# Performance work log

Measured on AMD Instinct MI355X. Metric: run time of the kernel, lower is better.

## Reference

```python
import jax, jax.numpy as jnp
import numpy as np

B, N1, N2, H, LAT, MID = 16, 2048, 2048, 768, 128, 256


def setup_inputs() -> dict:
    key = jax.random.key(0)
    ks = jax.random.split(key, 20)
    def lin(k, n_in, n_out):
        s = 1.0 / np.sqrt(n_in)
        kw, kb = jax.random.split(k)
        W = jax.random.uniform(kw, (n_in, n_out), jnp.float32, -s, s)
        b = jax.random.uniform(kb, (n_out,), jnp.float32, -s, s)
        return W, b
    We1, be1 = lin(ks[0], H, MID)
    We2, be2 = lin(ks[1], MID, LAT)
    Wq, bq = lin(ks[2], LAT, LAT)
    Wk, bk = lin(ks[3], LAT, LAT)
    Wv, bv = lin(ks[4], LAT, LAT)
    Wd1, bd1 = lin(ks[5], LAT, MID)
    Wd2, bd2 = lin(ks[6], MID, H)
    main_feature = jax.random.normal(ks[7], (B, N1, H), jnp.float32)
    feature = jax.random.normal(ks[8], (B, N2, H), jnp.float32)
    return dict(main_feature=main_feature, feature=feature,
                We1=We1, be1=be1, We2=We2, be2=be2,
                Wq=Wq, bq=bq, Wk=Wk, bk=bk, Wv=Wv, bv=bv,
                Wd1=Wd1, bd1=bd1, Wd2=Wd2, bd2=bd2)


def reference(main_feature, feature, We1, be1, We2, be2, Wq, bq, Wk, bk, Wv, bv, Wd1, bd1, Wd2, bd2):
    def encode(x):
        h = jax.nn.relu(x @ We1 + be1)
        return jax.nn.relu(h @ We2 + be2)  # [B, N, LAT]

    def decode(x):
        h = jax.nn.relu(x @ Wd1 + bd1)
        return jax.nn.sigmoid(h @ Wd2 + bd2)  # [B, N, H]

    m = encode(main_feature)           # [B, N1, LAT]
    f = encode(feature)                # [B, N2, LAT]
    q = m @ Wq + bq                    # [B, N1, LAT]
    k = f @ Wk + bk                    # [B, N2, LAT]
    v = f @ Wv + bv                    # [B, N2, LAT]
    scores = jnp.einsum('bnd,bmd->bnm', q, k)   # unscaled, [B, N1, N2]
    probs = jax.nn.softmax(scores, axis=-1)
    attn = jnp.einsum('bnm,bmd->bnd', probs, v)  # [B, N1, LAT]
    return decode(attn)                # [B, N1, H]
```

## Files before the change

kernel.cpp:

```cpp
#include <hip/hip_runtime.h>
#include <stdint.h>

typedef unsigned short u16;
typedef __bf16 bf16x8 __attribute__((ext_vector_type(8)));
typedef float f32x4 __attribute__((ext_vector_type(4)));

#define MM   32768

__device__ __forceinline__ u16 f2bf(float f) {
    uint32_t u; __builtin_memcpy(&u, &f, 4);
    u += 0x7fffu + ((u >> 16) & 1u);
    return (u16)(u >> 16);
}

__device__ __forceinline__ void gl_lds16(const u16* g, u16* l) {
    __builtin_amdgcn_global_load_lds(
        (__attribute__((address_space(1))) void*)(g),
        (__attribute__((address_space(3))) void*)(l), 16, 0, 0);
}

__global__ void transpose_all(const float* __restrict__ We1, const float* __restrict__ We2,
                              const float* __restrict__ Wq,  const float* __restrict__ Wk,
                              const float* __restrict__ Wv,  const float* __restrict__ Wd1,
                              const float* __restrict__ Wd2, u16* __restrict__ wt) {
    int i = blockIdx.x * 256 + threadIdx.x;
    const float* src; int K, N, off;
    if      (i < 196608) { src = We1; K = 768; N = 256; off = i;          }
    else if (i < 229376) { src = We2; K = 256; N = 128; off = i - 196608; }
    else if (i < 245760) { src = Wq;  K = 128; N = 128; off = i - 229376; }
    else if (i < 262144) { src = Wk;  K = 128; N = 128; off = i - 245760; }
    else if (i < 278528) { src = Wv;  K = 128; N = 128; off = i - 262144; }
    else if (i < 311296) { src = Wd1; K = 128; N = 256; off = i - 278528; }
    else if (i < 507904) { src = Wd2; K = 256; N = 768; off = i - 311296; }
    else return;
    int n = off / K, k = off % K;
    wt[i] = f2bf(src[(size_t)k * N + n]);
}

template <int BM, int ACT, bool TRANS, bool A_F32, bool OUT_F32>
__global__ void gemm_bt(const void* __restrict__ Avp, const u16* __restrict__ Wt,
                        const float* __restrict__ bias, void* __restrict__ Cvp,
                        int M, int N, int K) {
    constexpr int MI  = BM / 32;
    constexpr int AF4 = BM / 16;
    __shared__ u16 a_sh[2][BM * 64];
    __shared__ u16 b_sh[2][128 * 64];
    const int t = threadIdx.x;
    const int wave = t >> 6, lane = t & 63;
    const int lrow = lane & 15, quad = lane >> 4;
    const int wr = wave >> 1, wc = wave & 1;
    const int m0 = blockIdx.x * BM, n0 = blockIdx.y * 128;

    const float* Af = (const float*)Avp;
    const u16*   Ab = (const u16*)Avp;

    f32x4 acc[MI][4];
#pragma unroll
    for (int i = 0; i < MI; i++)
#pragma unroll
        for (int j = 0; j < 4; j++) acc[i][j] = (f32x4){0.f, 0.f, 0.f, 0.f};

    float4 pf[A_F32 ? AF4 : 1];

    auto stage_b = [&](int buf, int k0) {
#pragma unroll
        for (int it = 0; it < 4; it++) {
            int s = it * 256 + t;
            gl_lds16(Wt + (size_t)(n0 + (s >> 3)) * K + k0 + (s & 7) * 8,
                     &b_sh[buf][(it * 256 + wave * 64) * 8]);
        }
    };
    auto stage_a_bf = [&](int buf, int k0) {
#pragma unroll
        for (int it = 0; it < BM / 32; it++) {
            int s = it * 256 + t;
            gl_lds16(Ab + (size_t)(m0 + (s >> 3)) * K + k0 + (s & 7) * 8,
                     &a_sh[buf][(it * 256 + wave * 64) * 8]);
        }
    };
    auto load_a_f32 = [&](int k0) {
#pragma unroll
        for (int it = 0; it < AF4; it++) {
            int s = it * 256 + t;
            pf[it] = *(const float4*)(Af + (size_t)(m0 + (s >> 4)) * K + k0 + (s & 15) * 4);
        }
    };
    auto write_a_f32 = [&](int buf) {
#pragma unroll
        for (int it = 0; it < AF4; it++) {
            int s = it * 256 + t;
            int row = s >> 4, kc = s & 15;
            float4 v = pf[it];
            uint32_t p0 = (uint32_t)f2bf(v.x) | ((uint32_t)f2bf(v.y) << 16);
            uint32_t p1 = (uint32_t)f2bf(v.z) | ((uint32_t)f2bf(v.w) << 16);
            *(uint32_t*)&a_sh[buf][row * 64 + kc * 4]     = p0;
            *(uint32_t*)&a_sh[buf][row * 64 + kc * 4 + 2] = p1;
        }
    };

    if (A_F32) { load_a_f32(0); write_a_f32(0); } else stage_a_bf(0, 0);
    stage_b(0, 0);
    __syncthreads();

    int cur = 0;
    for (int k0 = 0; k0 < K; k0 += 64) {
        const int nk = k0 + 64;
        if (nk < K) {
            if (A_F32) load_a_f32(nk); else stage_a_bf(cur ^ 1, nk);
            stage_b(cur ^ 1, nk);
        }
#pragma unroll
        for (int kk = 0; kk < 2; kk++) {
            bf16x8 af[MI], bfv[4];
#pragma unroll
            for (int i = 0; i < MI; i++)
                af[i] = *(const bf16x8*)&a_sh[cur][(wr * (BM / 2) + i * 16 + lrow) * 64 + kk * 32 + quad * 8];
#pragma unroll
            for (int j = 0; j < 4; j++)
                bfv[j] = *(const bf16x8*)&b_sh[cur][(wc * 64 + j * 16 + lrow) * 64 + kk * 32 + quad * 8];
#pragma unroll
            for (int i = 0; i < MI; i++)
#pragma unroll
                for (int j = 0; j < 4; j++)
                    acc[i][j] = __builtin_amdgcn_mfma_f32_16x16x32_bf16(af[i], bfv[j], acc[i][j], 0, 0, 0);
        }
        if (A_F32 && nk < K) write_a_f32(cur ^ 1);
        __syncthreads();
        cur ^= 1;
    }

    float bv4[4];
#pragma unroll
    for (int j = 0; j < 4; j++) bv4[j] = bias[n0 + wc * 64 + j * 16 + lrow];

#pragma unroll
    for (int i = 0; i < MI; i++) {
#pragma unroll
        for (int j = 0; j < 4; j++) {
            const int col = n0 + wc * 64 + j * 16 + lrow;
            if (!TRANS) {
#pragma unroll
                for (int r = 0; r < 4; r++) {
                    float x = acc[i][j][r] + bv4[j];
                    if (ACT == 1) x = fmaxf(x, 0.f);
                    if (ACT == 2) x = 1.f / (1.f + __expf(-x));
                    const int row = m0 + wr * (BM / 2) + i * 16 + quad * 4 + r;
                    if (OUT_F32) ((float*)Cvp)[(size_t)row * N + col] = x;
                    else         ((u16*)Cvp)[(size_t)row * N + col] = f2bf(x);
                }
            } else {
                u16 vv[4];
#pragma unroll
                for (int r = 0; r < 4; r++) vv[r] = f2bf(acc[i][j][r] + bv4[j]);
                u16* Cb = (u16*)Cvp;
                size_t base = (size_t)(m0 >> 11) * ((size_t)N * 2048) + (size_t)col * 2048 +
                              (m0 & 2047) + wr * (BM / 2) + i * 16 + quad * 4;
                *(uint32_t*)&Cb[base]     = (uint32_t)vv[0] | ((uint32_t)vv[1] << 16);
                *(uint32_t*)&Cb[base + 2] = (uint32_t)vv[2] | ((uint32_t)vv[3] << 16);
            }
        }
    }
}

__global__ __launch_bounds__(256)
void flash_attn(const u16* __restrict__ Q, const u16* __restrict__ Kb,
                const u16* __restrict__ VT, u16* __restrict__ O) {
    __shared__ u16 k_sh[64 * 128];
    __shared__ u16 v_sh[128 * 64];
    __shared__ u16 qp_sh[64 * 128];

    const int t = threadIdx.x, wave = t >> 6, lane = t & 63;
    const int lrow = lane & 15, quad = lane >> 4;
    const int lsw = (lrow & 7) << 3;
    const int b = blockIdx.x >> 5, q0 = (blockIdx.x & 31) * 64;

    const u16* qg = Q + (size_t)(b * 2048 + q0) * 128;
#pragma unroll
    for (int it = 0; it < 4; it++) {
        int s = it * 256 + t;
        int srcSeg = s ^ ((s >> 4) & 7);
        gl_lds16(qg + (size_t)srcSeg * 8, &qp_sh[(it * 256 + wave * 64) * 8]);
    }
    __syncthreads();
    bf16x8 qf[4];
#pragma unroll
    for (int ks = 0; ks < 4; ks++)
        qf[ks] = *(const bf16x8*)&qp_sh[(((wave * 16 + lrow) * 128) + ks * 32 + quad * 8) ^ lsw];

    f32x4 o_acc[8];
#pragma unroll
    for (int ct = 0; ct < 8; ct++) o_acc[ct] = (f32x4){0.f, 0.f, 0.f, 0.f};
    float m_i[4] = {-1e30f, -1e30f, -1e30f, -1e30f};
    float l_i[4] = {0.f, 0.f, 0.f, 0.f};

    for (int tile = 0; tile < 32; tile++) {
        const u16* kg = Kb + (size_t)(b * 2048 + tile * 64) * 128;
        const u16* vg = VT + (size_t)b * 262144 + tile * 64;
#pragma unroll
        for (int it = 0; it < 4; it++) {
            int s = it * 256 + t;
            int srcSeg = s ^ ((s >> 4) & 7);
            gl_lds16(kg + (size_t)srcSeg * 8, &k_sh[(it * 256 + wave * 64) * 8]);
        }
#pragma unroll
        for (int it = 0; it < 4; it++) {
            int s = it * 256 + t;
            int row = s >> 3, c = (s & 7) ^ (row & 7);
            gl_lds16(vg + (size_t)row * 2048 + c * 8,
                     &v_sh[(it * 256 + wave * 64) * 8]);
        }
        __syncthreads();

        f32x4 s_acc[4];
        __builtin_amdgcn_s_setprio(1);
#pragma unroll
        for (int ct = 0; ct < 4; ct++) {
            f32x4 a = (f32x4){0.f, 0.f, 0.f, 0.f};
#pragma unroll
            for (int ks = 0; ks < 4; ks++) {
                bf16x8 kf = *(const bf16x8*)&k_sh[(((ct * 16 + lrow) * 128) + ks * 32 + quad * 8) ^ lsw];
                a = __builtin_amdgcn_mfma_f32_16x16x32_bf16(qf[ks], kf, a, 0, 0, 0);
            }
            s_acc[ct] = a;
        }
        __builtin_amdgcn_s_setprio(0);

        float mnew[4], alpha[4], ps[4];
#pragma unroll
        for (int r = 0; r < 4; r++) {
            float mx = s_acc[0][r];
#pragma unroll
            for (int ct = 1; ct < 4; ct++) mx = fmaxf(mx, s_acc[ct][r]);
#pragma unroll
            for (int d = 8; d >= 1; d >>= 1) mx = fmaxf(mx, __shfl_xor(mx, d, 64));
            mnew[r] = fmaxf(m_i[r], mx);
            alpha[r] = __expf(m_i[r] - mnew[r]);
            m_i[r] = mnew[r];
            ps[r] = 0.f;
        }
#pragma unroll
        for (int ct = 0; ct < 4; ct++)
#pragma unroll
            for (int r = 0; r < 4; r++) {
                float p = __expf(s_acc[ct][r] - mnew[r]);
                ps[r] += p;
                qp_sh[(((wave * 16 + quad * 4 + r) * 128) + ct * 16 + lrow) ^ (((quad * 4 + r) & 7) << 3)] = f2bf(p);
            }
#pragma unroll
        for (int r = 0; r < 4; r++) {
#pragma unroll
            for (int d = 8; d >= 1; d >>= 1) ps[r] += __shfl_xor(ps[r], d, 64);
            l_i[r] = l_i[r] * alpha[r] + ps[r];
        }
#pragma unroll
        for (int ct = 0; ct < 8; ct++)
#pragma unroll
            for (int r = 0; r < 4; r++) o_acc[ct][r] *= alpha[r];

        bf16x8 pf[2];
#pragma unroll
        for (int ks = 0; ks < 2; ks++)
            pf[ks] = *(const bf16x8*)&qp_sh[(((wave * 16 + lrow) * 128) + ks * 32 + quad * 8) ^ lsw];
        __builtin_amdgcn_s_setprio(1);
#pragma unroll
        for (int ct = 0; ct < 8; ct++)
#pragma unroll
            for (int ks = 0; ks < 2; ks++) {
                bf16x8 vf = *(const bf16x8*)&v_sh[(((ct * 16 + lrow) * 64) + ks * 32 + quad * 8) ^ lsw];
                o_acc[ct] = __builtin_amdgcn_mfma_f32_16x16x32_bf16(pf[ks], vf, o_acc[ct], 0, 0, 0);
            }
        __builtin_amdgcn_s_setprio(0);
        __syncthreads();
    }

    float inv_l[4];
#pragma unroll
    for (int r = 0; r < 4; r++) inv_l[r] = 1.f / l_i[r];
#pragma unroll
    for (int ct = 0; ct < 8; ct++)
#pragma unroll
        for (int r = 0; r < 4; r++) {
            const int row = b * 2048 + q0 + wave * 16 + quad * 4 + r;
            O[(size_t)row * 128 + ct * 16 + lrow] = f2bf(o_acc[ct][r] * inv_l[r]);
        }
}

extern "C" void kernel_launch(void* const* d_in, const int* in_sizes, int n_in,
                              void* d_out, int out_size, void* d_ws, size_t ws_size,
                              hipStream_t stream) {
    const float* mainf = (const float*)d_in[0];
    const float* feat  = (const float*)d_in[1];
    const float* We1 = (const float*)d_in[2];  const float* be1 = (const float*)d_in[3];
    const float* We2 = (const float*)d_in[4];  const float* be2 = (const float*)d_in[5];
    const float* Wq  = (const float*)d_in[6];  const float* bq  = (const float*)d_in[7];
    const float* Wk  = (const float*)d_in[8];  const float* bk  = (const float*)d_in[9];
    const float* Wv  = (const float*)d_in[10]; const float* bv  = (const float*)d_in[11];
    const float* Wd1 = (const float*)d_in[12]; const float* bd1 = (const float*)d_in[13];
    const float* Wd2 = (const float*)d_in[14]; const float* bd2 = (const float*)d_in[15];

    u16* ws = (u16*)d_ws;
    u16* wt = ws;
    u16* h1 = wt + 524288;
    u16* mf = h1 + 8388608;
    u16* qb = mf + 4194304;
    u16* kb = qb + 4194304;
    u16* vT = kb + 4194304;
    u16* wt_e1 = wt, *wt_e2 = wt + 196608, *wt_q = wt + 229376, *wt_k = wt + 245760,
       * wt_v = wt + 262144, *wt_d1 = wt + 278528, *wt_d2 = wt + 311296;

    transpose_all<<<1984, 256, 0, stream>>>(We1, We2, Wq, Wk, Wv, Wd1, Wd2, wt);

    gemm_bt<64, 1, false, true,  false><<<dim3(512, 2), 256, 0, stream>>>(mainf, wt_e1, be1, h1, MM, 256, 768);
    gemm_bt<64, 1, false, false, false><<<dim3(512, 1), 256, 0, stream>>>(h1,    wt_e2, be2, mf, MM, 128, 256);
    gemm_bt<64, 0, false, false, false><<<dim3(512, 1), 256, 0, stream>>>(mf,    wt_q,  bq,  qb, MM, 128, 128);
    gemm_bt<64, 1, false, true,  false><<<dim3(512, 2), 256, 0, stream>>>(feat, wt_e1, be1, h1, MM, 256, 768);
    gemm_bt<64, 1, false, false, false><<<dim3(512, 1), 256, 0, stream>>>(h1,   wt_e2, be2, mf, MM, 128, 256);
    gemm_bt<64, 0, false, false, false><<<dim3(512, 1), 256, 0, stream>>>(mf,   wt_k,  bk,  kb, MM, 128, 128);
    gemm_bt<64, 0, true,  false, false><<<dim3(512, 1), 256, 0, stream>>>(mf,   wt_v,  bv,  vT, MM, 128, 128);

    flash_attn<<<512, 256, 0, stream>>>(qb, kb, vT, mf);

    gemm_bt<64, 1, false, false, false><<<dim3(512, 2), 256, 0, stream>>>(mf, wt_d1, bd1, h1, MM, 256, 128);
    gemm_bt<64, 2, false, false, true ><<<dim3(512, 6), 256, 0, stream>>>(h1, wt_d2, bd2, d_out, MM, 768, 256);
}
```

Baseline: 496.1 us.

## Double-buffer K tiles in flash attention and use fine-grained vmcnt waits in GEMM

The flash attention kernel now double-buffers the K tile and prefetches the next K tile, plus the next V tile, while the current tile is being computed. Explicit s_waitcnt vmcnt counts and raw barriers replace __syncthreads. The GEMM main loop is restructured the same way, with partial vmcnt waits so the next tile's global loads overlap the MFMA compute, and setprio is raised around the MFMA block. This targets load latency exposed at each barrier, at the cost of more LDS and fragile hand-tuned wait counts that can cause races if they are wrong.

```diff
diff --git a/kernel.cpp b/kernel.cpp
--- a/kernel.cpp
+++ b/kernel.cpp
@@ -6,6 +6,11 @@
 typedef float f32x4 __attribute__((ext_vector_type(4)));
 
 #define MM   32768
+
+#define WAITV(N) asm volatile("s_waitcnt vmcnt(" #N ")" ::: "memory")
+#define WAITL0() asm volatile("s_waitcnt lgkmcnt(0)" ::: "memory")
+#define BARR()   do { asm volatile("" ::: "memory"); __builtin_amdgcn_s_barrier(); \
+                      asm volatile("" ::: "memory"); } while (0)
 
 __device__ __forceinline__ u16 f2bf(float f) {
     uint32_t u; __builtin_memcpy(&u, &f, 4);
@@ -97,35 +102,58 @@
             *(uint32_t*)&a_sh[buf][row * 64 + kc * 4 + 2] = p1;
         }
     };
-
-    if (A_F32) { load_a_f32(0); write_a_f32(0); } else stage_a_bf(0, 0);
-    stage_b(0, 0);
-    __syncthreads();
+    auto compute = [&](int buf) {
+#pragma unroll
+        for (int kk = 0; kk < 2; kk++) {
+            bf16x8 af[MI], bfv[4];
+#pragma unroll
+            for (int i = 0; i < MI; i++)
+                af[i] = *(const bf16x8*)&a_sh[buf][(wr * (BM / 2) + i * 16 + lrow) * 64 + kk * 32 + quad * 8];
+#pragma unroll
+            for (int j = 0; j < 4; j++)
+                bfv[j] = *(const bf16x8*)&b_sh[buf][(wc * 64 + j * 16 + lrow) * 64 + kk * 32 + quad * 8];
+            __builtin_amdgcn_s_setprio(1);
+#pragma unroll
+            for (int i = 0; i < MI; i++)
+#pragma unroll
+                for (int j = 0; j < 4; j++)
+                    acc[i][j] = __builtin_amdgcn_mfma_f32_16x16x32_bf16(af[i], bfv[j], acc[i][j], 0, 0, 0);
+            __builtin_amdgcn_s_setprio(0);
+        }
+    };
+
+    const int T = K >> 6;
+    if (A_F32) {
+        load_a_f32(0); stage_b(0, 0);
+        WAITV(4);
+        write_a_f32(0);
+        WAITL0(); WAITV(0);
+    } else {
+        stage_a_bf(0, 0); stage_b(0, 0);
+        WAITV(0);
+    }
+    BARR();
 
     int cur = 0;
-    for (int k0 = 0; k0 < K; k0 += 64) {
-        const int nk = k0 + 64;
-        if (nk < K) {
+    for (int tt = 0; tt < T; ++tt) {
+        const int nk = (tt + 1) * 64;
+        const bool more = nk < K;
+        if (more) {
             if (A_F32) load_a_f32(nk); else stage_a_bf(cur ^ 1, nk);
             stage_b(cur ^ 1, nk);
         }
-#pragma unroll
-        for (int kk = 0; kk < 2; kk++) {
-            bf16x8 af[MI], bfv[4];
-#pragma unroll
-            for (int i = 0; i < MI; i++)
-                af[i] = *(const bf16x8*)&a_sh[cur][(wr * (BM / 2) + i * 16 + lrow) * 64 + kk * 32 + quad * 8];
-#pragma unroll
-            for (int j = 0; j < 4; j++)
-                bfv[j] = *(const bf16x8*)&b_sh[cur][(wc * 64 + j * 16 + lrow) * 64 + kk * 32 + quad * 8];
-#pragma unroll
-            for (int i = 0; i < MI; i++)
-#pragma unroll
-                for (int j = 0; j < 4; j++)
-                    acc[i][j] = __builtin_amdgcn_mfma_f32_16x16x32_bf16(af[i], bfv[j], acc[i][j], 0, 0, 0);
-        }
-        if (A_F32 && nk < K) write_a_f32(cur ^ 1);
-        __syncthreads();
+        if (tt > 0) {
+            if (more) { if (A_F32) { WAITV(8); } else { WAITV(6); } }
+            else      { WAITV(0); }
+            BARR();
+        }
+        compute(cur);
+        if (A_F32 && more) {
+            WAITV(4);
+            write_a_f32(cur ^ 1);
+            WAITL0();
+        }
+        if (more) BARR();
         cur ^= 1;
     }
 
@@ -165,7 +193,7 @@
 __global__ __launch_bounds__(256)
 void flash_attn(const u16* __restrict__ Q, const u16* __restrict__ Kb,
                 const u16* __restrict__ VT, u16* __restrict__ O) {
-    __shared__ u16 k_sh[64 * 128];
+    __shared__ u16 kb_sh[2][64 * 128];
     __shared__ u16 v_sh[128 * 64];
     __shared__ u16 qp_sh[64 * 128];
 
@@ -174,14 +202,27 @@
     const int lsw = (lrow & 7) << 3;
     const int b = blockIdx.x >> 5, q0 = (blockIdx.x & 31) * 64;
 
-    const u16* qg = Q + (size_t)(b * 2048 + q0) * 128;
+    int ksrc[4], vsrc[4], ldst[4];
 #pragma unroll
     for (int it = 0; it < 4; it++) {
         int s = it * 256 + t;
-        int srcSeg = s ^ ((s >> 4) & 7);
-        gl_lds16(qg + (size_t)srcSeg * 8, &qp_sh[(it * 256 + wave * 64) * 8]);
-    }
-    __syncthreads();
+        ksrc[it] = (s ^ ((s >> 4) & 7)) * 8;
+        int row = s >> 3, cc = (s & 7) ^ (row & 7);
+        vsrc[it] = row * 2048 + cc * 8;
+        ldst[it] = (it * 256 + wave * 64) * 8;
+    }
+
+    const u16* qg  = Q  + (size_t)(b * 2048 + q0) * 128;
+    const u16* kgb = Kb + (size_t)b * 2048 * 128;
+    const u16* vgb = VT + (size_t)b * 262144;
+
+#pragma unroll
+    for (int it = 0; it < 4; it++) gl_lds16(qg + ksrc[it], &qp_sh[ldst[it]]);
+#pragma unroll
+    for (int it = 0; it < 4; it++) gl_lds16(kgb + ksrc[it], &kb_sh[0][ldst[it]]);
+#pragma unroll
+    for (int it = 0; it < 4; it++) gl_lds16(vgb + vsrc[it], &v_sh[ldst[it]]);
+    WAITV(8); BARR();
     bf16x8 qf[4];
 #pragma unroll
     for (int ks = 0; ks < 4; ks++)
@@ -194,22 +235,11 @@
     float l_i[4] = {0.f, 0.f, 0.f, 0.f};
 
     for (int tile = 0; tile < 32; tile++) {
-        const u16* kg = Kb + (size_t)(b * 2048 + tile * 64) * 128;
-        const u16* vg = VT + (size_t)b * 262144 + tile * 64;
-#pragma unroll
-        for (int it = 0; it < 4; it++) {
-            int s = it * 256 + t;
-            int srcSeg = s ^ ((s >> 4) & 7);
-            gl_lds16(kg + (size_t)srcSeg * 8, &k_sh[(it * 256 + wave * 64) * 8]);
-        }
-#pragma unroll
-        for (int it = 0; it < 4; it++) {
-            int s = it * 256 + t;
-            int row = s >> 3, c = (s & 7) ^ (row & 7);
-            gl_lds16(vg + (size_t)row * 2048 + c * 8,
-                     &v_sh[(it * 256 + wave * 64) * 8]);
-        }
-        __syncthreads();
+        const int c = tile & 1;
+        const u16* kg_n = kgb + (size_t)(((tile + 1) & 31) * 64) * 128;
+#pragma unroll
+        for (int it = 0; it < 4; it++) gl_lds16(kg_n + ksrc[it], &kb_sh[c ^ 1][ldst[it]]);
+        WAITV(8); BARR();
 
         f32x4 s_acc[4];
         __builtin_amdgcn_s_setprio(1);
@@ -218,7 +248,7 @@
             f32x4 a = (f32x4){0.f, 0.f, 0.f, 0.f};
 #pragma unroll
             for (int ks = 0; ks < 4; ks++) {
-                bf16x8 kf = *(const bf16x8*)&k_sh[(((ct * 16 + lrow) * 128) + ks * 32 + quad * 8) ^ lsw];
+                bf16x8 kf = *(const bf16x8*)&kb_sh[c][(((ct * 16 + lrow) * 128) + ks * 32 + quad * 8) ^ lsw];
                 a = __builtin_amdgcn_mfma_f32_16x16x32_bf16(qf[ks], kf, a, 0, 0, 0);
             }
             s_acc[ct] = a;
@@ -257,20 +287,28 @@
 #pragma unroll
             for (int r = 0; r < 4; r++) o_acc[ct][r] *= alpha[r];
 
-        bf16x8 pf[2];
+        WAITV(4); BARR();
+
+        bf16x8 pfa[2];
 #pragma unroll
         for (int ks = 0; ks < 2; ks++)
-            pf[ks] = *(const bf16x8*)&qp_sh[(((wave * 16 + lrow) * 128) + ks * 32 + quad * 8) ^ lsw];
+            pfa[ks] = *(const bf16x8*)&qp_sh[(((wave * 16 + lrow) * 128) + ks * 32 + quad * 8) ^ lsw];
         __builtin_amdgcn_s_setprio(1);
 #pragma unroll
         for (int ct = 0; ct < 8; ct++)
 #pragma unroll
             for (int ks = 0; ks < 2; ks++) {
                 bf16x8 vf = *(const bf16x8*)&v_sh[(((ct * 16 + lrow) * 64) + ks * 32 + quad * 8) ^ lsw];
-                o_acc[ct] = __builtin_amdgcn_mfma_f32_16x16x32_bf16(pf[ks], vf, o_acc[ct], 0, 0, 0);
+                o_acc[ct] = __builtin_amdgcn_mfma_f32_16x16x32_bf16(pfa[ks], vf, o_acc[ct], 0, 0, 0);
             }
         __builtin_amdgcn_s_setprio(0);
-        __syncthreads();
+
+        if (tile < 31) {
+            BARR();
+            const u16* vg_n = vgb + (tile + 1) * 64;
+#pragma unroll
+            for (int it = 0; it < 4; it++) gl_lds16(vg_n + vsrc[it], &v_sh[ldst[it]]);
+        }
     }
 
     float inv_l[4];
```

Result: no change. 498.5 us (+0.5%).
